# Kernel optimization log

Measured on AMD Instinct MI355X. Metric: run time of the kernel, lower is better.

Reference implementation:

```python
import jax, jax.numpy as jnp
import numpy as np

NUM_BINS = 32
SIGMA_RATIO = 1.0
SMOOTH_NR = 1e-7
SMOOTH_DR = 1e-7


def _parzen_weights(x, bin_centers, preterm):
    # x: [B, N]; returns normalized Gaussian Parzen weights [B, N, K]
    d = x[..., None] - bin_centers  # [B, N, K]
    w = jnp.exp(-preterm * d * d)
    return w / jnp.sum(w, axis=-1, keepdims=True)


def _mi_loss(pred, target):
    B = pred.shape[0]
    p = pred.reshape(B, -1)  # [B, N]
    t = target.reshape(B, -1)
    N = p.shape[1]

    # min/max are detached (.item() in torch); images in [0,1] use fixed range (0,1)
    minval = jax.lax.stop_gradient(jnp.minimum(p.min(), t.min()))
    maxval = jax.lax.stop_gradient(jnp.maximum(p.max(), t.max()))
    in_range = (maxval <= 1.0) & (minval >= 0.0)
    minval = jnp.where(in_range, jnp.float32(0.0), minval)
    maxval = jnp.where(in_range, jnp.float32(1.0), maxval)

    bin_centers = minval + (maxval - minval) * jnp.linspace(0.0, 1.0, NUM_BINS, dtype=p.dtype)  # [K]
    sigma = (maxval - minval) / (NUM_BINS - 1) * SIGMA_RATIO
    preterm = 1.0 / (2.0 * sigma * sigma)

    wa = _parzen_weights(p, bin_centers, preterm)  # [B, N, K]
    wb = _parzen_weights(t, bin_centers, preterm)  # [B, N, K]

    pa = jnp.mean(wa, axis=1)  # [B, K] == pa of shape B,1,K squeezed
    pb = jnp.mean(wb, axis=1)  # [B, K]
    pab = jnp.einsum('bnk,bnl->bkl', wa, wb) / N  # [B, K, K] joint histogram
    papb = pa[:, :, None] * pb[:, None, :]  # [B, K, K] outer product == bmm(pa^T, pb)

    mi = jnp.sum(pab * jnp.log((pab + SMOOTH_NR) / (papb + SMOOTH_DR) + SMOOTH_DR), axis=(-1, -2))  # [B]
    return -jnp.mean(mi)  # reduction='mean', negated


def setup_inputs() -> dict:
    key = jax.random.key(0)
    k1, k2 = jax.random.split(key)
    shape = (1, 1, 128, 128, 128)
    pred = jax.random.uniform(k1, shape, dtype=jnp.float32)
    target = jax.random.uniform(k2, shape, dtype=jnp.float32)
    return {"pred": pred, "target": target}


def reference(pred, target):
    return _mi_loss(pred, target)
```

## Files before the change

kernel.cpp:

```cpp
#include <hip/hip_runtime.h>
#include <math.h>

#ifndef __has_builtin
#define __has_builtin(x) 0
#endif
#if __has_builtin(__builtin_amdgcn_exp2f)
#define EXP2F(x) __builtin_amdgcn_exp2f(x)
#else
#define EXP2F(x) exp2f(x)
#endif
#if __has_builtin(__builtin_amdgcn_rcpf)
#define RCPF(x) __builtin_amdgcn_rcpf(x)
#else
#define RCPF(x) (1.0f / (x))
#endif

typedef _Float16 f16x8 __attribute__((ext_vector_type(8)));
typedef _Float16 h2 __attribute__((ext_vector_type(2)));
typedef float f32x4 __attribute__((ext_vector_type(4)));

union Frag {
  f16x8 v;
  h2 p[4];
};

__device__ __forceinline__ h2 pkrtz(float a, float b) {
#if __has_builtin(__builtin_amdgcn_cvt_pkrtz)
  return __builtin_bit_cast(h2, __builtin_amdgcn_cvt_pkrtz(a, b));
#else
  h2 r; r.x = (_Float16)a; r.y = (_Float16)b; return r;
#endif
}

__device__ __forceinline__ float trunc16(float w) {
  return __builtin_bit_cast(float, __builtin_bit_cast(unsigned int, w) & 0xFFFFE000u);
}

constexpr int KBINS = 32;
constexpr int MM_BLOCKS = 512;
constexpr int MAIN_BLOCKS = 1024;
constexpr int NTHR = 512;
constexpr int WPB = 8;
constexpr int BATCH = 32;
constexpr int NSLOT = 64;
constexpr int ACC_OFF_F = 4096;

#define MFMA16(a, b, c) __builtin_amdgcn_mfma_f32_16x16x32_f16((a), (b), (c), 0, 0, 0)

template <int CTRL>
__device__ __forceinline__ float rot_add(float v) {
  int r = __builtin_amdgcn_update_dpp(0, __builtin_bit_cast(int, v), CTRL, 0xF, 0xF, true);
  return v + __builtin_bit_cast(float, r);
}
__device__ __forceinline__ float row_sum16(float v) {
  v = rot_add<0x128>(v);
  v = rot_add<0x124>(v);
  v = rot_add<0x122>(v);
  v = rot_add<0x121>(v);
  return v;
}

__device__ __forceinline__ void eraw(float x, float c0, float c1, float npl2,
                                     float& e0, float& e1, float& s) {
  float d0 = x - c0, d1 = x - c1;
  e0 = EXP2F((npl2 * d0) * d0);
  e1 = EXP2F((npl2 * d1) * d1);
  s = row_sum16(e0 + e1);
}

__global__ __launch_bounds__(256) void k_minmax(const float* __restrict__ p,
                                                const float* __restrict__ t,
                                                int n, float* __restrict__ ws) {
  int tid = blockIdx.x * 256 + threadIdx.x;
  int nth = gridDim.x * 256;
  if (tid < NSLOT * 1024) ((double*)(ws + ACC_OFF_F))[tid] = 0.0;

  float mn = INFINITY, mx = -INFINITY;
  int n4 = n >> 2;
  const float4* p4 = (const float4*)p;
  const float4* t4 = (const float4*)t;
  for (int i = tid; i < n4; i += nth) {
    float4 a = p4[i];
    mn = fminf(mn, fminf(fminf(a.x, a.y), fminf(a.z, a.w)));
    mx = fmaxf(mx, fmaxf(fmaxf(a.x, a.y), fmaxf(a.z, a.w)));
    float4 b = t4[i];
    mn = fminf(mn, fminf(fminf(b.x, b.y), fminf(b.z, b.w)));
    mx = fmaxf(mx, fmaxf(fmaxf(b.x, b.y), fmaxf(b.z, b.w)));
  }
  for (int i = (n4 << 2) + tid; i < n; i += nth) {
    mn = fminf(mn, fminf(p[i], t[i]));
    mx = fmaxf(mx, fmaxf(p[i], t[i]));
  }
  for (int off = 32; off; off >>= 1) {
    mn = fminf(mn, __shfl_xor(mn, off, 64));
    mx = fmaxf(mx, __shfl_xor(mx, off, 64));
  }
  __shared__ float smn[4], smx[4];
  int wv = threadIdx.x >> 6;
  if ((threadIdx.x & 63) == 0) { smn[wv] = mn; smx[wv] = mx; }
  __syncthreads();
  if (threadIdx.x == 0) {
    mn = fminf(fminf(smn[0], smn[1]), fminf(smn[2], smn[3]));
    mx = fmaxf(fmaxf(smx[0], smx[1]), fmaxf(smx[2], smx[3]));
    ws[16 + 2 * blockIdx.x] = mn;
    ws[17 + 2 * blockIdx.x] = mx;
  }
}

__global__ __launch_bounds__(NTHR, 4) void k_main(const float* __restrict__ p,
                                                  const float* __restrict__ t,
                                                  int n, float* __restrict__ ws) {
  __shared__ __align__(16) float red[WPB][KBINS * KBINS];
  __shared__ float s_par[4];

  const int tidx = threadIdx.x;
  const int lane = tidx & 63;
  const int wv = tidx >> 6;

  if (tidx < 64) {
    float mn = INFINITY, mx = -INFINITY;
    for (int b = lane; b < MM_BLOCKS; b += 64) {
      mn = fminf(mn, ws[16 + 2 * b]);
      mx = fmaxf(mx, ws[17 + 2 * b]);
    }
    for (int off = 32; off; off >>= 1) {
      mn = fminf(mn, __shfl_xor(mn, off, 64));
      mx = fmaxf(mx, __shfl_xor(mx, off, 64));
    }
    if (lane == 0) {
      bool in_range = (mx <= 1.0f) && (mn >= 0.0f);
      float minv = in_range ? 0.0f : mn;
      float maxv = in_range ? 1.0f : mx;
      float drange = maxv - minv;
      float sigma = drange * (1.0f / (KBINS - 1));
      float preterm = 1.0f / (2.0f * sigma * sigma);
      s_par[0] = minv;
      s_par[1] = drange * (1.0f / (KBINS - 1));
      s_par[2] = preterm * 1.44269504088896340736f;
    }
  }
  __syncthreads();
  const float minv = s_par[0], delta = s_par[1];
  const float npl2 = -s_par[2];

  const int m = lane & 15;
  const int quad = lane >> 4;
  const int qb = quad << 3;
  const float c0 = fmaf(delta, (float)m, minv);
  const float c1 = fmaf(delta, (float)(m + 16), minv);

  f32x4 acc00 = {0.f, 0.f, 0.f, 0.f};
  f32x4 acc01 = {0.f, 0.f, 0.f, 0.f};
  f32x4 acc10 = {0.f, 0.f, 0.f, 0.f};
  f32x4 acc11 = {0.f, 0.f, 0.f, 0.f};

  const int per_wave = n >> 13;
  const int base = (blockIdx.x * WPB + wv) * per_wave;

  for (int it = 0; it < per_wave; it += BATCH) {
    const int sbase = base + it + qb;
    float4 a0 = *(const float4*)(p + sbase);
    float4 a1 = *(const float4*)(p + sbase + 4);
    float4 b0 = *(const float4*)(t + sbase);
    float4 b1 = *(const float4*)(t + sbase + 4);
    float xa[8] = {a0.x, a0.y, a0.z, a0.w, a1.x, a1.y, a1.z, a1.w};
    float xb[8] = {b0.x, b0.y, b0.z, b0.w, b1.x, b1.y, b1.z, b1.w};

    Frag Ah0, Al0, Ah1, Al1, Bh0, Bl0, Bh1, Bl1;
#pragma unroll
    for (int jp = 0; jp < 4; ++jp) {
      float ea00, ea01, sa0, ea10, ea11, sa1;
      float eb00, eb01, sb0, eb10, eb11, sb1;
      eraw(xa[2 * jp],     c0, c1, npl2, ea00, ea01, sa0);
      eraw(xa[2 * jp + 1], c0, c1, npl2, ea10, ea11, sa1);
      eraw(xb[2 * jp],     c0, c1, npl2, eb00, eb01, sb0);
      eraw(xb[2 * jp + 1], c0, c1, npl2, eb10, eb11, sb1);
      float pr0 = sa0 * sb0;
      float i0 = RCPF(pr0);
      i0 = i0 * fmaf(-pr0, i0, 2.0f);
      i0 *= 4096.0f;
      float pr1 = sa1 * sb1;
      float i1 = RCPF(pr1);
      i1 = i1 * fmaf(-pr1, i1, 2.0f);
      i1 *= 4096.0f;
      float wa00 = ea00 * i0, wa01 = ea01 * i0;
      float wa10 = ea10 * i1, wa11 = ea11 * i1;
      float wb00 = eb00 * 64.0f, wb01 = eb01 * 64.0f;
      float wb10 = eb10 * 64.0f, wb11 = eb11 * 64.0f;
      float H;
      H = trunc16(wa00); float la00 = wa00 - H; float ha00 = H;
      H = trunc16(wa10); float la10 = wa10 - H; float ha10 = H;
      H = trunc16(wa01); float la01 = wa01 - H; float ha01 = H;
      H = trunc16(wa11); float la11 = wa11 - H; float ha11 = H;
      H = trunc16(wb00); float lb00 = wb00 - H; float hb00 = H;
      H = trunc16(wb10); float lb10 = wb10 - H; float hb10 = H;
      H = trunc16(wb01); float lb01 = wb01 - H; float hb01 = H;
      H = trunc16(wb11); float lb11 = wb11 - H; float hb11 = H;
      Ah0.p[jp] = pkrtz(ha00, ha10);
      Ah1.p[jp] = pkrtz(ha01, ha11);
      Bh0.p[jp] = pkrtz(hb00, hb10);
      Bh1.p[jp] = pkrtz(hb01, hb11);
      Al0.p[jp] = h2{(_Float16)la00, (_Float16)la10};
      Al1.p[jp] = h2{(_Float16)la01, (_Float16)la11};
      Bl0.p[jp] = h2{(_Float16)lb00, (_Float16)lb10};
      Bl1.p[jp] = h2{(_Float16)lb01, (_Float16)lb11};
    }
    acc00 = MFMA16(Ah0.v, Bh0.v, acc00);
    acc01 = MFMA16(Ah0.v, Bh1.v, acc01);
    acc10 = MFMA16(Ah1.v, Bh0.v, acc10);
    acc11 = MFMA16(Ah1.v, Bh1.v, acc11);
    acc00 = MFMA16(Al0.v, Bh0.v, acc00);
    acc01 = MFMA16(Al0.v, Bh1.v, acc01);
    acc10 = MFMA16(Al1.v, Bh0.v, acc10);
    acc11 = MFMA16(Al1.v, Bh1.v, acc11);
    acc00 = MFMA16(Ah0.v, Bl0.v, acc00);
    acc01 = MFMA16(Ah0.v, Bl1.v, acc01);
    acc10 = MFMA16(Ah1.v, Bl0.v, acc10);
    acc11 = MFMA16(Ah1.v, Bl1.v, acc11);
    acc00 = MFMA16(Al0.v, Bl0.v, acc00);
    acc01 = MFMA16(Al0.v, Bl1.v, acc01);
    acc10 = MFMA16(Al1.v, Bl0.v, acc10);
    acc11 = MFMA16(Al1.v, Bl1.v, acc11);
  }

#pragma unroll
  for (int reg = 0; reg < 4; ++reg) {
    int r0 = quad * 4 + reg;
    red[wv][r0 * KBINS + m] = acc00[reg];
    red[wv][r0 * KBINS + 16 + m] = acc01[reg];
    red[wv][(16 + r0) * KBINS + m] = acc10[reg];
    red[wv][(16 + r0) * KBINS + 16 + m] = acc11[reg];
  }
  __syncthreads();
  {
    int c = 2 * tidx;
    float s0 = 0.f, s1 = 0.f;
#pragma unroll
    for (int w = 0; w < WPB; ++w) {
      float2 v = *(const float2*)&red[w][c];
      s0 += v.x;
      s1 += v.y;
    }
    double* acc = (double*)(ws + ACC_OFF_F) + (size_t)(blockIdx.x & (NSLOT - 1)) * 1024;
    unsafeAtomicAdd(&acc[c], (double)s0);
    unsafeAtomicAdd(&acc[c + 1], (double)s1);
  }
}

__global__ __launch_bounds__(1024) void k_final(const float* __restrict__ ws_f,
                                                float* __restrict__ out, int n) {
  const double* acc = (const double*)(ws_f + ACC_OFF_F);
  __shared__ double pab_s[1024];
  __shared__ double pa_s[32], pb_s[32];
  __shared__ double wsum[16];
  int tid = threadIdx.x;
  double s0 = 0.0, s1 = 0.0, s2 = 0.0, s3 = 0.0;
#pragma unroll
  for (int slot = 0; slot < NSLOT; slot += 4) {
    s0 += acc[(size_t)(slot + 0) * 1024 + tid];
    s1 += acc[(size_t)(slot + 1) * 1024 + tid];
    s2 += acc[(size_t)(slot + 2) * 1024 + tid];
    s3 += acc[(size_t)(slot + 3) * 1024 + tid];
  }
  double s = (s0 + s1) + (s2 + s3);
  double pab = s / ((double)n * 262144.0);
  pab_s[tid] = pab;
  __syncthreads();
  if (tid < 32) {
    double a = 0.0;
    for (int l = 0; l < 32; ++l) a += pab_s[tid * 32 + l];
    pa_s[tid] = a;
  } else if (tid < 64) {
    int l = tid - 32;
    double b = 0.0;
    for (int k2 = 0; k2 < 32; ++k2) b += pab_s[k2 * 32 + l];
    pb_s[l] = b;
  }
  __syncthreads();
  int k = tid >> 5, l = tid & 31;
  double papb = pa_s[k] * pb_s[l];
  double v = pab * log((pab + 1e-7) / (papb + 1e-7) + 1e-7);
  for (int off = 32; off; off >>= 1) v += __shfl_down(v, off, 64);
  if ((tid & 63) == 0) wsum[tid >> 6] = v;
  __syncthreads();
  if (tid < 64) {
    double w = (tid < 16) ? wsum[tid] : 0.0;
    for (int off = 8; off; off >>= 1) w += __shfl_down(w, off, 64);
    if (tid == 0) out[0] = (float)(-w);
  }
}

extern "C" void kernel_launch(void* const* d_in, const int* in_sizes, int n_in,
                              void* d_out, int out_size, void* d_ws, size_t ws_size,
                              hipStream_t stream) {
  const float* p = (const float*)d_in[0];
  const float* t = (const float*)d_in[1];
  float* out = (float*)d_out;
  float* ws = (float*)d_ws;
  int n = in_sizes[0];

  k_minmax<<<dim3(MM_BLOCKS), dim3(256), 0, stream>>>(p, t, n, ws);
  k_main<<<dim3(MAIN_BLOCKS), dim3(NTHR), 0, stream>>>(p, t, n, ws);
  k_final<<<dim3(1), dim3(1024), 0, stream>>>(ws, out, n);
}
```

Measured before the change: 132.1 us.

## Fuse final reduction into main kernel via last-block counter and interleave DPP sums

```diff
diff --git a/kernel.cpp b/kernel.cpp
--- a/kernel.cpp
+++ b/kernel.cpp
@@ -52,21 +52,6 @@
   int r = __builtin_amdgcn_update_dpp(0, __builtin_bit_cast(int, v), CTRL, 0xF, 0xF, true);
   return v + __builtin_bit_cast(float, r);
 }
-__device__ __forceinline__ float row_sum16(float v) {
-  v = rot_add<0x128>(v);
-  v = rot_add<0x124>(v);
-  v = rot_add<0x122>(v);
-  v = rot_add<0x121>(v);
-  return v;
-}
-
-__device__ __forceinline__ void eraw(float x, float c0, float c1, float npl2,
-                                     float& e0, float& e1, float& s) {
-  float d0 = x - c0, d1 = x - c1;
-  e0 = EXP2F((npl2 * d0) * d0);
-  e1 = EXP2F((npl2 * d1) * d1);
-  s = row_sum16(e0 + e1);
-}
 
 __global__ __launch_bounds__(256) void k_minmax(const float* __restrict__ p,
                                                 const float* __restrict__ t,
@@ -74,6 +59,7 @@
   int tid = blockIdx.x * 256 + threadIdx.x;
   int nth = gridDim.x * 256;
   if (tid < NSLOT * 1024) ((double*)(ws + ACC_OFF_F))[tid] = 0.0;
+  if (tid == 0) ((unsigned*)ws)[0] = 0u;
 
   float mn = INFINITY, mx = -INFINITY;
   int n4 = n >> 2;
@@ -109,9 +95,13 @@
 
 __global__ __launch_bounds__(NTHR, 4) void k_main(const float* __restrict__ p,
                                                   const float* __restrict__ t,
-                                                  int n, float* __restrict__ ws) {
+                                                  int n, float* __restrict__ ws,
+                                                  float* __restrict__ out) {
   __shared__ __align__(16) float red[WPB][KBINS * KBINS];
   __shared__ float s_par[4];
+  __shared__ int s_last;
+  __shared__ double pa_s[KBINS], pb_s[KBINS];
+  __shared__ double fsum[WPB];
 
   const int tidx = threadIdx.x;
   const int lane = tidx & 63;
@@ -169,12 +159,31 @@
     Frag Ah0, Al0, Ah1, Al1, Bh0, Bl0, Bh1, Bl1;
 #pragma unroll
     for (int jp = 0; jp < 4; ++jp) {
-      float ea00, ea01, sa0, ea10, ea11, sa1;
-      float eb00, eb01, sb0, eb10, eb11, sb1;
-      eraw(xa[2 * jp],     c0, c1, npl2, ea00, ea01, sa0);
-      eraw(xa[2 * jp + 1], c0, c1, npl2, ea10, ea11, sa1);
-      eraw(xb[2 * jp],     c0, c1, npl2, eb00, eb01, sb0);
-      eraw(xb[2 * jp + 1], c0, c1, npl2, eb10, eb11, sb1);
+      const float x0 = xa[2 * jp], x1 = xa[2 * jp + 1];
+      const float y0 = xb[2 * jp], y1 = xb[2 * jp + 1];
+      float dA00 = x0 - c0, dA01 = x0 - c1;
+      float dA10 = x1 - c0, dA11 = x1 - c1;
+      float dB00 = y0 - c0, dB01 = y0 - c1;
+      float dB10 = y1 - c0, dB11 = y1 - c1;
+      float gA00 = (npl2 * dA00) * dA00, gA01 = (npl2 * dA01) * dA01;
+      float gA10 = (npl2 * dA10) * dA10, gA11 = (npl2 * dA11) * dA11;
+      float gB00 = (npl2 * dB00) * dB00, gB01 = (npl2 * dB01) * dB01;
+      float gB10 = (npl2 * dB10) * dB10, gB11 = (npl2 * dB11) * dB11;
+      float ea00 = EXP2F(gA00), ea01 = EXP2F(gA01);
+      float ea10 = EXP2F(gA10), ea11 = EXP2F(gA11);
+      float eb00 = EXP2F(gB00), eb01 = EXP2F(gB01);
+      float eb10 = EXP2F(gB10), eb11 = EXP2F(gB11);
+      float r0 = ea00 + ea01, r1 = ea10 + ea11;
+      float r2 = eb00 + eb01, r3 = eb10 + eb11;
+      r0 = rot_add<0x128>(r0); r1 = rot_add<0x128>(r1);
+      r2 = rot_add<0x128>(r2); r3 = rot_add<0x128>(r3);
+      r0 = rot_add<0x124>(r0); r1 = rot_add<0x124>(r1);
+      r2 = rot_add<0x124>(r2); r3 = rot_add<0x124>(r3);
+      r0 = rot_add<0x122>(r0); r1 = rot_add<0x122>(r1);
+      r2 = rot_add<0x122>(r2); r3 = rot_add<0x122>(r3);
+      r0 = rot_add<0x121>(r0); r1 = rot_add<0x121>(r1);
+      r2 = rot_add<0x121>(r2); r3 = rot_add<0x121>(r3);
+      const float sa0 = r0, sa1 = r1, sb0 = r2, sb1 = r3;
       float pr0 = sa0 * sb0;
       float i0 = RCPF(pr0);
       i0 = i0 * fmaf(-pr0, i0, 2.0f);
@@ -245,48 +254,57 @@
     unsafeAtomicAdd(&acc[c], (double)s0);
     unsafeAtomicAdd(&acc[c + 1], (double)s1);
   }
-}
-
-__global__ __launch_bounds__(1024) void k_final(const float* __restrict__ ws_f,
-                                                float* __restrict__ out, int n) {
-  const double* acc = (const double*)(ws_f + ACC_OFF_F);
-  __shared__ double pab_s[1024];
-  __shared__ double pa_s[32], pb_s[32];
-  __shared__ double wsum[16];
-  int tid = threadIdx.x;
-  double s0 = 0.0, s1 = 0.0, s2 = 0.0, s3 = 0.0;
+
+  __threadfence();
+  if (tidx == 0) {
+    unsigned old = atomicAdd((unsigned*)ws, 1u);
+    s_last = (old == MAIN_BLOCKS - 1) ? 1 : 0;
+  }
+  __syncthreads();
+  if (!s_last) return;
+  __threadfence();
+
+  double* pd = (double*)&red[0][0];
+  const double* acc = (const double*)(ws + ACC_OFF_F);
+  for (int c = tidx; c < 1024; c += NTHR) {
+    double s0 = 0.0, s1 = 0.0, s2 = 0.0, s3 = 0.0;
 #pragma unroll
-  for (int slot = 0; slot < NSLOT; slot += 4) {
-    s0 += acc[(size_t)(slot + 0) * 1024 + tid];
-    s1 += acc[(size_t)(slot + 1) * 1024 + tid];
-    s2 += acc[(size_t)(slot + 2) * 1024 + tid];
-    s3 += acc[(size_t)(slot + 3) * 1024 + tid];
-  }
-  double s = (s0 + s1) + (s2 + s3);
-  double pab = s / ((double)n * 262144.0);
-  pab_s[tid] = pab;
-  __syncthreads();
-  if (tid < 32) {
+    for (int slot = 0; slot < NSLOT; slot += 4) {
+      s0 += acc[(size_t)(slot + 0) * 1024 + c];
+      s1 += acc[(size_t)(slot + 1) * 1024 + c];
+      s2 += acc[(size_t)(slot + 2) * 1024 + c];
+      s3 += acc[(size_t)(slot + 3) * 1024 + c];
+    }
+    double s = (s0 + s1) + (s2 + s3);
+    pd[c] = s / ((double)n * 262144.0);
+  }
+  __syncthreads();
+  if (tidx < 32) {
     double a = 0.0;
-    for (int l = 0; l < 32; ++l) a += pab_s[tid * 32 + l];
-    pa_s[tid] = a;
-  } else if (tid < 64) {
-    int l = tid - 32;
+    for (int l = 0; l < 32; ++l) a += pd[tidx * 32 + l];
+    pa_s[tidx] = a;
+  } else if (tidx < 64) {
+    int l = tidx - 32;
     double b = 0.0;
-    for (int k2 = 0; k2 < 32; ++k2) b += pab_s[k2 * 32 + l];
+    for (int k2 = 0; k2 < 32; ++k2) b += pd[k2 * 32 + l];
     pb_s[l] = b;
   }
   __syncthreads();
-  int k = tid >> 5, l = tid & 31;
-  double papb = pa_s[k] * pb_s[l];
-  double v = pab * log((pab + 1e-7) / (papb + 1e-7) + 1e-7);
-  for (int off = 32; off; off >>= 1) v += __shfl_down(v, off, 64);
-  if ((tid & 63) == 0) wsum[tid >> 6] = v;
-  __syncthreads();
-  if (tid < 64) {
-    double w = (tid < 16) ? wsum[tid] : 0.0;
-    for (int off = 8; off; off >>= 1) w += __shfl_down(w, off, 64);
-    if (tid == 0) out[0] = (float)(-w);
+  {
+    double v = 0.0;
+    for (int c = tidx; c < 1024; c += NTHR) {
+      double pab = pd[c];
+      double papb = pa_s[c >> 5] * pb_s[c & 31];
+      v += pab * log((pab + 1e-7) / (papb + 1e-7) + 1e-7);
+    }
+    for (int off = 32; off; off >>= 1) v += __shfl_down(v, off, 64);
+    if ((tidx & 63) == 0) fsum[wv] = v;
+    __syncthreads();
+    if (tidx == 0) {
+      double tot = 0.0;
+      for (int w = 0; w < WPB; ++w) tot += fsum[w];
+      out[0] = (float)(-tot);
+    }
   }
 }
 
@@ -300,6 +318,5 @@
   int n = in_sizes[0];
 
   k_minmax<<<dim3(MM_BLOCKS), dim3(256), 0, stream>>>(p, t, n, ws);
-  k_main<<<dim3(MAIN_BLOCKS), dim3(NTHR), 0, stream>>>(p, t, n, ws);
-  k_final<<<dim3(1), dim3(1024), 0, stream>>>(ws, out, n);
-}
+  k_main<<<dim3(MAIN_BLOCKS), dim3(NTHR), 0, stream>>>(p, t, n, ws, out);
+}
```

Result: slower. 246.4 us (+86.4%).
